# Kernel tuning notes

Hardware: AMD Instinct MI355X
Metric: run time of the kernel (lower is better)

The kernel has to match this reference:

```python
import jax, jax.numpy as jnp
import numpy as np

NUM_ITER = 3
SLOT_DIM = 16
INPUT_DIM = 256
HIDDEN_DIM = 128
EPS = 1e-8
LN_EPS = 1e-5  # torch LayerNorm default


def _layernorm(x, w, b):
    mu = jnp.mean(x, axis=-1, keepdims=True)
    var = jnp.mean((x - mu) ** 2, axis=-1, keepdims=True)
    return (x - mu) * jax.lax.rsqrt(var + LN_EPS) * w + b


def setup_inputs() -> dict:
    key = jax.random.key(0)
    ks = jax.random.split(key, 12)
    B, N, K = 32, 4096, 8
    D, S, H = INPUT_DIM, SLOT_DIM, HIDDEN_DIM
    inputs = jax.random.normal(ks[0], (B, N, D), dtype=jnp.float32)
    init_slots = jax.random.normal(ks[1], (B, K, S), dtype=jnp.float32)
    return {
        "inputs": inputs,
        "init_slots": init_slots,
        "ln_in_w": jnp.ones((D,), jnp.float32),
        "ln_in_b": jnp.zeros((D,), jnp.float32),
        "ln_s_w": jnp.ones((S,), jnp.float32),
        "ln_s_b": jnp.zeros((S,), jnp.float32),
        "ln_m_w": jnp.ones((S,), jnp.float32),
        "ln_m_b": jnp.zeros((S,), jnp.float32),
        "wq": jax.random.normal(ks[2], (S, S), jnp.float32) * (S ** -0.5),
        "wk": jax.random.normal(ks[3], (S, D), jnp.float32) * (D ** -0.5),
        "wv": jax.random.normal(ks[4], (S, D), jnp.float32) * (D ** -0.5),
        "w_ih": jax.random.normal(ks[5], (3 * S, S), jnp.float32) * (S ** -0.5),
        "w_hh": jax.random.normal(ks[6], (3 * S, S), jnp.float32) * (S ** -0.5),
        "b_ih": jnp.zeros((3 * S,), jnp.float32),
        "b_hh": jnp.zeros((3 * S,), jnp.float32),
        "mlp_w1": jax.random.normal(ks[7], (H, S), jnp.float32) * (S ** -0.5),
        "mlp_b1": jnp.zeros((H,), jnp.float32),
        "mlp_w2": jax.random.normal(ks[8], (S, H), jnp.float32) * (H ** -0.5),
        "mlp_b2": jnp.zeros((S,), jnp.float32),
    }


def _gru_cell(x, h, w_ih, w_hh, b_ih, b_hh):
    # torch GRUCell: gates ordered [r, z, n]
    gi = x @ w_ih.T + b_ih            # [BK, 3S]
    gh = h @ w_hh.T + b_hh
    i_r, i_z, i_n = jnp.split(gi, 3, axis=-1)
    h_r, h_z, h_n = jnp.split(gh, 3, axis=-1)
    r = jax.nn.sigmoid(i_r + h_r)
    z = jax.nn.sigmoid(i_z + h_z)
    n = jnp.tanh(i_n + r * h_n)
    return (1.0 - z) * n + z * h


def reference(inputs, init_slots, ln_in_w, ln_in_b, ln_s_w, ln_s_b, ln_m_w, ln_m_b,
              wq, wk, wv, w_ih, w_hh, b_ih, b_hh, mlp_w1, mlp_b1, mlp_w2, mlp_b2):
    B, N, _ = inputs.shape
    K = init_slots.shape[1]
    scale = SLOT_DIM ** -0.5

    x = _layernorm(inputs, ln_in_w, ln_in_b)
    k = jnp.einsum('bnd,sd->bns', x, wk)   # [B,N,S]
    v = jnp.einsum('bnd,sd->bns', x, wv)

    slots = init_slots
    attn = None
    for _ in range(NUM_ITER):
        slots_prev = slots
        q = jnp.einsum('bks,ts->bkt', _layernorm(slots, ln_s_w, ln_s_b), wq)
        logits = jnp.einsum('bks,bns->bkn', q, k) * scale       # [B,K,N]
        attn = jax.nn.softmax(logits, axis=1) + EPS              # softmax over SLOTS
        attn = attn / jnp.sum(attn, axis=-1, keepdims=True)
        updates = jnp.einsum('bkn,bns->bks', attn, v)            # [B,K,S]
        h = _gru_cell(updates.reshape(B * K, -1), slots_prev.reshape(B * K, -1),
                      w_ih, w_hh, b_ih, b_hh).reshape(B, K, -1)
        y = _layernorm(h, ln_m_w, ln_m_b)
        mlp = jax.nn.relu(y @ mlp_w1.T + mlp_b1) @ mlp_w2.T + mlp_b2
        slots = h + mlp
    return slots, attn
```

## Files before the change

kernel.cpp:

```cpp
#include <hip/hip_runtime.h>
#include <cstddef>


__device__ __forceinline__ float sigmoid_f(float x){ return 1.f/(1.f+__expf(-x)); }
__device__ __forceinline__ float tanh_f(float x){ return 1.f - 2.f/(__expf(2.f*x)+1.f); }

__global__ __launch_bounds__(256) void k_prep(
    const float* __restrict__ lnw, const float* __restrict__ lnb,
    const float* __restrict__ wk, const float* __restrict__ wv,
    const float* __restrict__ init_slots,
    const float* __restrict__ ln_s_w, const float* __restrict__ ln_s_b,
    const float* __restrict__ wq,
    float* __restrict__ wprepT, float* __restrict__ mt,
    float* __restrict__ qbuf, float* __restrict__ upd, float* __restrict__ Abuf,
    float* __restrict__ slots_out)
{
  int t = threadIdx.x;
  int i = blockIdx.x*256 + t;
  {
    int j = i & 15, s = (i >> 4) & 31, c = (i >> 9) & 3, p = i >> 11;
    int d = p*64 + c*16 + j;
    float w = (s < 16) ? wk[s*256+d] : wv[(s-16)*256+d];
    wprepT[i] = lnw[d]*w;
  }
  if (blockIdx.x != 0) return;
  {
    int s = t >> 3, j = t & 7;
    float m = 0.f, tv = 0.f;
    for (int d = j; d < 256; d += 8) {
      float w = (s < 16) ? wk[s*256+d] : wv[(s-16)*256+d];
      m  = fmaf(lnw[d], w, m);
      tv = fmaf(lnb[d], w, tv);
    }
    m += __shfl_xor(m,1);  m += __shfl_xor(m,2);  m += __shfl_xor(m,4);
    tv += __shfl_xor(tv,1); tv += __shfl_xor(tv,2); tv += __shfl_xor(tv,4);
    if (j == 0) { mt[s] = m; mt[32+s] = tv; }
  }
  #pragma unroll
  for (int j2 = 0; j2 < 16; ++j2) {
    slots_out[t*16+j2] = init_slots[t*16+j2];
    upd[t*16+j2] = 0.f;
  }
  Abuf[t] = 0.f;
  float sl[16];
  #pragma unroll
  for (int j2 = 0; j2 < 16; ++j2) sl[j2] = init_slots[t*16+j2];
  float mu = 0.f;
  #pragma unroll
  for (int j2 = 0; j2 < 16; ++j2) mu += sl[j2];
  mu *= (1.f/16.f);
  float var = 0.f;
  #pragma unroll
  for (int j2 = 0; j2 < 16; ++j2) { float d = sl[j2]-mu; var = fmaf(d,d,var); }
  var *= (1.f/16.f);
  float rstd = rsqrtf(var + 1e-5f);
  float y[16];
  #pragma unroll
  for (int j2 = 0; j2 < 16; ++j2) y[j2] = (sl[j2]-mu)*rstd*ln_s_w[j2] + ln_s_b[j2];
  #pragma unroll
  for (int tq = 0; tq < 16; ++tq) {
    float q = 0.f;
    #pragma unroll
    for (int s2 = 0; s2 < 16; ++s2) q = fmaf(y[s2], wq[tq*16+s2], q);
    qbuf[t*16+tq] = q;
  }
}

__global__ __launch_bounds__(256) void k_proj(
    const float* __restrict__ x, const float* __restrict__ wprepT,
    const float* __restrict__ mt,
    float* __restrict__ kout, float* __restrict__ vout)
{
  __shared__ float pbuf[4][64][35];
  int t = threadIdx.x;
  int lane = t & 63;
  int p = __builtin_amdgcn_readfirstlane(t >> 6);
  int row = blockIdx.x*64 + lane;
  const float* xr = x + (size_t)row*256 + p*64;
  const float* wp = wprepT + p*2048;

  float acc[32];
  #pragma unroll
  for (int s = 0; s < 32; ++s) acc[s] = 0.f;
  float sum = 0.f, sumsq = 0.f;

  float4 n0 = *(const float4*)(xr+0);
  float4 n1 = *(const float4*)(xr+4);
  float4 n2 = *(const float4*)(xr+8);
  float4 n3 = *(const float4*)(xr+12);
  #pragma unroll 1
  for (int c = 0; c < 4; ++c) {
    float4 x0 = n0, x1 = n1, x2 = n2, x3 = n3;
    if (c < 3) {
      const float* xn = xr + (c+1)*16;
      n0 = *(const float4*)(xn+0);
      n1 = *(const float4*)(xn+4);
      n2 = *(const float4*)(xn+8);
      n3 = *(const float4*)(xn+12);
    }
    float xe[16] = {x0.x,x0.y,x0.z,x0.w, x1.x,x1.y,x1.z,x1.w,
                    x2.x,x2.y,x2.z,x2.w, x3.x,x3.y,x3.z,x3.w};
    #pragma unroll
    for (int j = 0; j < 16; ++j) { sum += xe[j]; sumsq = fmaf(xe[j], xe[j], sumsq); }
    const float* wc = wp + c*512;
    #pragma unroll
    for (int s = 0; s < 32; ++s) {
      const float* w = wc + s*16;
      #pragma unroll
      for (int j = 0; j < 16; ++j) acc[s] = fmaf(xe[j], w[j], acc[s]);
    }
  }
  #pragma unroll
  for (int s = 0; s < 32; ++s) pbuf[p][lane][s] = acc[s];
  pbuf[p][lane][32] = sum;
  pbuf[p][lane][33] = sumsq;
  __syncthreads();

  int g = t >> 6, r = t & 63;
  float ts = 0.f, tq = 0.f;
  #pragma unroll
  for (int pp = 0; pp < 4; ++pp) { ts += pbuf[pp][r][32]; tq += pbuf[pp][r][33]; }
  float mu = ts*(1.f/256.f);
  float var = tq*(1.f/256.f) - mu*mu;
  float rstd = rsqrtf(var + 1e-5f);
  float o[8];
  #pragma unroll
  for (int j = 0; j < 8; ++j) {
    int a = g*8 + j;
    float v = 0.f;
    #pragma unroll
    for (int pp = 0; pp < 4; ++pp) v += pbuf[pp][r][a];
    o[j] = fmaf(rstd, v - mu*mt[a], mt[32+a]);
  }
  float* dst = ((g < 2) ? kout : vout) + (size_t)(blockIdx.x*64 + r)*16 + (g & 1)*8;
  *(float4*)(dst+0) = make_float4(o[0],o[1],o[2],o[3]);
  *(float4*)(dst+4) = make_float4(o[4],o[5],o[6],o[7]);
}

__global__ __launch_bounds__(256) void k_attn(
    const float* __restrict__ kproj, const float* __restrict__ vproj,
    const float* __restrict__ qbuf,
    float* __restrict__ upd, float* __restrict__ Abuf,
    float* __restrict__ attn_out, int write_attn)
{
  __shared__ float qs[128];
  __shared__ float ptile[8*257];
  __shared__ float vtile[16*257];
  int b = blockIdx.x >> 4;
  int n0 = (blockIdx.x & 15) * 256;
  int t = threadIdx.x;
  if (t < 128) qs[t] = qbuf[b*128 + t];

  float kv[16];
  {
    const float* kr = kproj + ((size_t)(b*4096 + n0 + t))*16;
    const float* vr = vproj + ((size_t)(b*4096 + n0 + t))*16;
    #pragma unroll
    for (int j = 0; j < 16; j += 4) {
      float4 f = *(const float4*)(kr+j);
      kv[j]=f.x; kv[j+1]=f.y; kv[j+2]=f.z; kv[j+3]=f.w;
      float4 g = *(const float4*)(vr+j);
      vtile[(j+0)*257+t]=g.x; vtile[(j+1)*257+t]=g.y;
      vtile[(j+2)*257+t]=g.z; vtile[(j+3)*257+t]=g.w;
    }
  }
  __syncthreads();
  {
    float lg[8];
    #pragma unroll
    for (int kk = 0; kk < 8; ++kk) {
      float a = 0.f;
      #pragma unroll
      for (int s = 0; s < 16; ++s) a = fmaf(qs[kk*16+s], kv[s], a);
      lg[kk] = a*0.25f;
    }
    float mx = lg[0];
    #pragma unroll
    for (int kk = 1; kk < 8; ++kk) mx = fmaxf(mx, lg[kk]);
    float se = 0.f;
    #pragma unroll
    for (int kk = 0; kk < 8; ++kk) { lg[kk] = __expf(lg[kk]-mx); se += lg[kk]; }
    float inv = 1.f/se;
    #pragma unroll
    for (int kk = 0; kk < 8; ++kk) {
      float pv = fmaf(lg[kk], inv, 1e-8f);
      ptile[kk*257 + t] = pv;
      if (write_attn) attn_out[((size_t)(b*8+kk))*4096 + n0 + t] = pv;
    }
  }
  __syncthreads();
  {
    int kk = t >> 5, r = t & 31, s = r >> 1, half = r & 1;
    const float* pr = ptile + kk*257 + half*128;
    const float* vr = vtile + s*257 + half*128;
    float acc = 0.f, asum = 0.f;
    #pragma unroll 8
    for (int i = 0; i < 128; ++i) {
      float pv = pr[i];
      asum += pv;
      acc = fmaf(pv, vr[i], acc);
    }
    acc  += __shfl_xor(acc, 1);
    asum += __shfl_xor(asum, 1);
    if (half == 0) {
      atomicAdd(upd + (b*8+kk)*16 + s, acc);
      if (s == 0) atomicAdd(Abuf + b*8 + kk, asum);
    }
  }
}

__global__ __launch_bounds__(256) void k_gru(
    float* __restrict__ upd, float* __restrict__ Abuf,
    float* __restrict__ slots, float* __restrict__ qbuf,
    const float* __restrict__ w_ih, const float* __restrict__ w_hh,
    const float* __restrict__ b_ih, const float* __restrict__ b_hh,
    const float* __restrict__ mlp_w1, const float* __restrict__ mlp_b1,
    const float* __restrict__ mlp_w2, const float* __restrict__ mlp_b2,
    const float* __restrict__ ln_m_w, const float* __restrict__ ln_m_b,
    const float* __restrict__ ln_s_w, const float* __restrict__ ln_s_b,
    const float* __restrict__ wq, int prep_next)
{
  __shared__ float s_wih[48*17], s_whh[48*17];
  __shared__ float s_bih[48], s_bhh[48];
  __shared__ float s_w1[128*17], s_b1[128];
  __shared__ float s_w2[16*129], s_b2[16];
  __shared__ float s_lnmw[16], s_lnmb[16], s_lnsw[16], s_lnsb[16];
  __shared__ float s_wq[16*17];
  int t = threadIdx.x;
  for (int i = t; i < 768; i += 256) {
    int g = i >> 4, j = i & 15;
    s_wih[g*17+j] = w_ih[i];
    s_whh[g*17+j] = w_hh[i];
  }
  for (int i = t; i < 2048; i += 256) {
    int r = i >> 4, c = i & 15;
    s_w1[r*17+c] = mlp_w1[i];
    int r2 = i >> 7, c2 = i & 127;
    s_w2[r2*129+c2] = mlp_w2[i];
  }
  if (t < 48) { s_bih[t] = b_ih[t]; s_bhh[t] = b_hh[t]; }
  if (t < 128) s_b1[t] = mlp_b1[t];
  if (t < 16) {
    s_b2[t] = mlp_b2[t];
    s_lnmw[t] = ln_m_w[t]; s_lnmb[t] = ln_m_b[t];
    s_lnsw[t] = ln_s_w[t]; s_lnsb[t] = ln_s_b[t];
  }
  for (int i = t; i < 256; i += 256) {
    int r = i >> 4, c = i & 15;
    s_wq[r*17+c] = wq[i];
  }
  __syncthreads();

  int bk = blockIdx.x*16 + (t >> 4);
  int s = t & 15;
  int laneBase = (t & 63) & ~15;

  float inv = 1.f / Abuf[bk];
  float u[16], h[16];
  #pragma unroll
  for (int j = 0; j < 16; ++j) {
    u[j] = upd[bk*16+j] * inv;
    h[j] = slots[bk*16+j];
  }
  float hs = slots[bk*16+s];

  float gir = s_bih[s],  giz = s_bih[16+s], gin = s_bih[32+s];
  float ghr = s_bhh[s],  ghz = s_bhh[16+s], ghn = s_bhh[32+s];
  #pragma unroll
  for (int j = 0; j < 16; ++j) {
    gir = fmaf(u[j], s_wih[s*17+j], gir);
    giz = fmaf(u[j], s_wih[(16+s)*17+j], giz);
    gin = fmaf(u[j], s_wih[(32+s)*17+j], gin);
    ghr = fmaf(h[j], s_whh[s*17+j], ghr);
    ghz = fmaf(h[j], s_whh[(16+s)*17+j], ghz);
    ghn = fmaf(h[j], s_whh[(32+s)*17+j], ghn);
  }
  float rr = sigmoid_f(gir + ghr);
  float zz = sigmoid_f(giz + ghz);
  float nn = tanh_f(gin + rr*ghn);
  float hn = (1.f-zz)*nn + zz*hs;

  float ssum = hn;
  #pragma unroll
  for (int m = 1; m < 16; m <<= 1) ssum += __shfl_xor(ssum, m);
  float mu = ssum*(1.f/16.f);
  float dv = hn - mu;
  float vs = dv*dv;
  #pragma unroll
  for (int m = 1; m < 16; m <<= 1) vs += __shfl_xor(vs, m);
  float rstd = rsqrtf(vs*(1.f/16.f) + 1e-5f);
  float y = dv*rstd*s_lnmw[s] + s_lnmb[s];

  float yv[16];
  #pragma unroll
  for (int j = 0; j < 16; ++j) yv[j] = __shfl(y, laneBase + j);

  float h1[8];
  #pragma unroll
  for (int i = 0; i < 8; ++i) {
    int jj = i*16 + s;
    float a = s_b1[jj];
    #pragma unroll
    for (int q = 0; q < 16; ++q) a = fmaf(yv[q], s_w1[jj*17+q], a);
    h1[i] = fmaxf(a, 0.f);
  }
  float o = s_b2[s];
  #pragma unroll
  for (int i = 0; i < 8; ++i) {
    #pragma unroll
    for (int sp = 0; sp < 16; ++sp) {
      float hv = __shfl(h1[i], laneBase + sp);
      o = fmaf(hv, s_w2[s*129 + i*16 + sp], o);
    }
  }
  float slot_new = hn + o;
  slots[bk*16+s] = slot_new;

  if (prep_next) {
    float ss = slot_new;
    #pragma unroll
    for (int m = 1; m < 16; m <<= 1) ss += __shfl_xor(ss, m);
    float mu2 = ss*(1.f/16.f);
    float d2 = slot_new - mu2;
    float v2 = d2*d2;
    #pragma unroll
    for (int m = 1; m < 16; m <<= 1) v2 += __shfl_xor(v2, m);
    float rstd2 = rsqrtf(v2*(1.f/16.f) + 1e-5f);
    float y2 = d2*rstd2*s_lnsw[s] + s_lnsb[s];
    float qv = 0.f;
    #pragma unroll
    for (int sp = 0; sp < 16; ++sp) qv = fmaf(__shfl(y2, laneBase+sp), s_wq[s*17+sp], qv);
    qbuf[bk*16+s] = qv;
    upd[bk*16+s] = 0.f;
    if (s == 0) Abuf[bk] = 0.f;
  }
}

__global__ __launch_bounds__(256) void k_scale(float* __restrict__ attn,
                                               const float* __restrict__ Abuf)
{
  int bk = blockIdx.x;
  float inv = 1.f / Abuf[bk];
  float4* p = (float4*)(attn + (size_t)bk*4096);
  #pragma unroll 4
  for (int i = threadIdx.x; i < 1024; i += 256) {
    float4 v = p[i];
    v.x *= inv; v.y *= inv; v.z *= inv; v.w *= inv;
    p[i] = v;
  }
}

extern "C" void kernel_launch(void* const* d_in, const int* in_sizes, int n_in,
                              void* d_out, int out_size, void* d_ws, size_t ws_size,
                              hipStream_t stream)
{
  const float* inputs     = (const float*)d_in[0];
  const float* init_slots = (const float*)d_in[1];
  const float* ln_in_w    = (const float*)d_in[2];
  const float* ln_in_b    = (const float*)d_in[3];
  const float* ln_s_w     = (const float*)d_in[4];
  const float* ln_s_b     = (const float*)d_in[5];
  const float* ln_m_w     = (const float*)d_in[6];
  const float* ln_m_b     = (const float*)d_in[7];
  const float* wq         = (const float*)d_in[8];
  const float* wk         = (const float*)d_in[9];
  const float* wv         = (const float*)d_in[10];
  const float* w_ih       = (const float*)d_in[11];
  const float* w_hh       = (const float*)d_in[12];
  const float* b_ih       = (const float*)d_in[13];
  const float* b_hh       = (const float*)d_in[14];
  const float* mlp_w1     = (const float*)d_in[15];
  const float* mlp_b1     = (const float*)d_in[16];
  const float* mlp_w2     = (const float*)d_in[17];
  const float* mlp_b2     = (const float*)d_in[18];

  float* ws    = (float*)d_ws;
  float* wprepT= ws;
  float* mt    = ws + 8192;
  float* qbuf  = ws + 8320;
  float* upd   = ws + 12416;
  float* Abuf  = ws + 16512;
  float* kproj = ws + 16768;
  float* vproj = kproj + 2097152;

  float* out   = (float*)d_out;
  float* slots = out;
  float* attn  = out + 4096;

  k_prep<<<32, 256, 0, stream>>>(ln_in_w, ln_in_b, wk, wv, init_slots,
                                 ln_s_w, ln_s_b, wq,
                                 wprepT, mt, qbuf, upd, Abuf, slots);
  k_proj<<<2048, 256, 0, stream>>>(inputs, wprepT, mt, kproj, vproj);
  for (int it = 0; it < 3; ++it) {
    int last = (it == 2);
    k_attn<<<512, 256, 0, stream>>>(kproj, vproj, qbuf, upd, Abuf, attn, last);
    k_gru<<<16, 256, 0, stream>>>(upd, Abuf, slots, qbuf,
                                  w_ih, w_hh, b_ih, b_hh,
                                  mlp_w1, mlp_b1, mlp_w2, mlp_b2,
                                  ln_m_w, ln_m_b, ln_s_w, ln_s_b,
                                  wq, last ? 0 : 1);
  }
  k_scale<<<256, 256, 0, stream>>>(attn, Abuf);
}
```

Before: 320.2 us.

## Stage input rows through LDS with coalesced loads in projection and attention kernels

The projection kernel now loads x tiles cooperatively with coalesced float4 reads into shared memory, double-buffered through registers, instead of having each thread stride its own row. The weight layout is reordered to match. The attention kernel stages k through an LDS tile with coalesced loads and vectorizes the dot products and the p·v reduction with float4 LDS reads using padded strides. This targets uncoalesced global access and scalar LDS traffic, at the cost of extra barriers per chunk.

```diff
diff --git a/kernel.cpp b/kernel.cpp
--- a/kernel.cpp
+++ b/kernel.cpp
@@ -18,8 +18,8 @@
   int t = threadIdx.x;
   int i = blockIdx.x*256 + t;
   {
-    int j = i & 15, s = (i >> 4) & 31, c = (i >> 9) & 3, p = i >> 11;
-    int d = p*64 + c*16 + j;
+    int j = i & 15, s = (i >> 4) & 31, g = i >> 9;
+    int d = g*16 + j;
     float w = (s < 16) ? wk[s*256+d] : wv[(s-16)*256+d];
     wprepT[i] = lnw[d]*w;
   }
@@ -71,55 +71,70 @@
     const float* __restrict__ mt,
     float* __restrict__ kout, float* __restrict__ vout)
 {
-  __shared__ float pbuf[4][64][35];
+  __shared__ float smem[8960];
+  float* xs = smem;
+  float* pb = smem;
   int t = threadIdx.x;
   int lane = t & 63;
   int p = __builtin_amdgcn_readfirstlane(t >> 6);
-  int row = blockIdx.x*64 + lane;
-  const float* xr = x + (size_t)row*256 + p*64;
-  const float* wp = wprepT + p*2048;
+  int r0 = blockIdx.x*64;
+  int srow = t >> 4, scol = (t & 15)*4;
 
   float acc[32];
   #pragma unroll
   for (int s = 0; s < 32; ++s) acc[s] = 0.f;
   float sum = 0.f, sumsq = 0.f;
 
-  float4 n0 = *(const float4*)(xr+0);
-  float4 n1 = *(const float4*)(xr+4);
-  float4 n2 = *(const float4*)(xr+8);
-  float4 n3 = *(const float4*)(xr+12);
+  float4 st[4];
+  #pragma unroll
+  for (int i = 0; i < 4; ++i)
+    st[i] = *(const float4*)(x + (size_t)(r0 + i*16 + srow)*256 + 0*64 + scol);
+  #pragma unroll
+  for (int i = 0; i < 4; ++i)
+    *(float4*)&xs[(i*16 + srow)*68 + scol] = st[i];
+  __syncthreads();
+
   #pragma unroll 1
   for (int c = 0; c < 4; ++c) {
-    float4 x0 = n0, x1 = n1, x2 = n2, x3 = n3;
     if (c < 3) {
-      const float* xn = xr + (c+1)*16;
-      n0 = *(const float4*)(xn+0);
-      n1 = *(const float4*)(xn+4);
-      n2 = *(const float4*)(xn+8);
-      n3 = *(const float4*)(xn+12);
-    }
-    float xe[16] = {x0.x,x0.y,x0.z,x0.w, x1.x,x1.y,x1.z,x1.w,
-                    x2.x,x2.y,x2.z,x2.w, x3.x,x3.y,x3.z,x3.w};
+      #pragma unroll
+      for (int i = 0; i < 4; ++i)
+        st[i] = *(const float4*)(x + (size_t)(r0 + i*16 + srow)*256 + (c+1)*64 + scol);
+    }
+    float xe[16];
+    #pragma unroll
+    for (int i = 0; i < 4; ++i) {
+      float4 f = *(const float4*)&xs[lane*68 + p*16 + i*4];
+      xe[i*4+0]=f.x; xe[i*4+1]=f.y; xe[i*4+2]=f.z; xe[i*4+3]=f.w;
+    }
     #pragma unroll
     for (int j = 0; j < 16; ++j) { sum += xe[j]; sumsq = fmaf(xe[j], xe[j], sumsq); }
-    const float* wc = wp + c*512;
+    const float* wc = wprepT + (c*4 + p)*512;
     #pragma unroll
     for (int s = 0; s < 32; ++s) {
       const float* w = wc + s*16;
       #pragma unroll
       for (int j = 0; j < 16; ++j) acc[s] = fmaf(xe[j], w[j], acc[s]);
     }
-  }
-  #pragma unroll
-  for (int s = 0; s < 32; ++s) pbuf[p][lane][s] = acc[s];
-  pbuf[p][lane][32] = sum;
-  pbuf[p][lane][33] = sumsq;
+    __syncthreads();
+    if (c < 3) {
+      #pragma unroll
+      for (int i = 0; i < 4; ++i)
+        *(float4*)&xs[(i*16 + srow)*68 + scol] = st[i];
+      __syncthreads();
+    }
+  }
+
+  #pragma unroll
+  for (int s = 0; s < 32; ++s) pb[(p*64 + lane)*35 + s] = acc[s];
+  pb[(p*64 + lane)*35 + 32] = sum;
+  pb[(p*64 + lane)*35 + 33] = sumsq;
   __syncthreads();
 
   int g = t >> 6, r = t & 63;
   float ts = 0.f, tq = 0.f;
   #pragma unroll
-  for (int pp = 0; pp < 4; ++pp) { ts += pbuf[pp][r][32]; tq += pbuf[pp][r][33]; }
+  for (int pp = 0; pp < 4; ++pp) { ts += pb[(pp*64+r)*35 + 32]; tq += pb[(pp*64+r)*35 + 33]; }
   float mu = ts*(1.f/256.f);
   float var = tq*(1.f/256.f) - mu*mu;
   float rstd = rsqrtf(var + 1e-5f);
@@ -129,10 +144,10 @@
     int a = g*8 + j;
     float v = 0.f;
     #pragma unroll
-    for (int pp = 0; pp < 4; ++pp) v += pbuf[pp][r][a];
+    for (int pp = 0; pp < 4; ++pp) v += pb[(pp*64+r)*35 + a];
     o[j] = fmaf(rstd, v - mu*mt[a], mt[32+a]);
   }
-  float* dst = ((g < 2) ? kout : vout) + (size_t)(blockIdx.x*64 + r)*16 + (g & 1)*8;
+  float* dst = ((g < 2) ? kout : vout) + (size_t)(r0 + r)*16 + (g & 1)*8;
   *(float4*)(dst+0) = make_float4(o[0],o[1],o[2],o[3]);
   *(float4*)(dst+4) = make_float4(o[4],o[5],o[6],o[7]);
 }
@@ -144,35 +159,50 @@
     float* __restrict__ attn_out, int write_attn)
 {
   __shared__ float qs[128];
-  __shared__ float ptile[8*257];
-  __shared__ float vtile[16*257];
+  __shared__ float ktile[256*20];
+  __shared__ float vtile[16*260];
+  __shared__ float ptile[8*260];
   int b = blockIdx.x >> 4;
   int n0 = (blockIdx.x & 15) * 256;
   int t = threadIdx.x;
+
+  const float* kbase = kproj + ((size_t)(b*4096 + n0))*16;
+  const float* vbase = vproj + ((size_t)(b*4096 + n0))*16;
+  {
+    int nn = t >> 2, s0 = (t & 3)*4;
+    #pragma unroll
+    for (int i = 0; i < 4; ++i) {
+      int n = i*64 + nn;
+      float4 kf = *(const float4*)(kbase + n*16 + s0);
+      *(float4*)&ktile[n*20 + s0] = kf;
+      float4 vf = *(const float4*)(vbase + n*16 + s0);
+      vtile[(s0+0)*260 + n] = vf.x;
+      vtile[(s0+1)*260 + n] = vf.y;
+      vtile[(s0+2)*260 + n] = vf.z;
+      vtile[(s0+3)*260 + n] = vf.w;
+    }
+  }
   if (t < 128) qs[t] = qbuf[b*128 + t];
-
-  float kv[16];
+  __syncthreads();
+
   {
-    const float* kr = kproj + ((size_t)(b*4096 + n0 + t))*16;
-    const float* vr = vproj + ((size_t)(b*4096 + n0 + t))*16;
-    #pragma unroll
-    for (int j = 0; j < 16; j += 4) {
-      float4 f = *(const float4*)(kr+j);
-      kv[j]=f.x; kv[j+1]=f.y; kv[j+2]=f.z; kv[j+3]=f.w;
-      float4 g = *(const float4*)(vr+j);
-      vtile[(j+0)*257+t]=g.x; vtile[(j+1)*257+t]=g.y;
-      vtile[(j+2)*257+t]=g.z; vtile[(j+3)*257+t]=g.w;
-    }
-  }
-  __syncthreads();
-  {
+    float4 kv[4];
+    #pragma unroll
+    for (int i = 0; i < 4; ++i) kv[i] = *(const float4*)&ktile[t*20 + i*4];
+    const float4* q4 = (const float4*)qs;
     float lg[8];
     #pragma unroll
     for (int kk = 0; kk < 8; ++kk) {
-      float a = 0.f;
+      float4 a4 = make_float4(0.f,0.f,0.f,0.f);
       #pragma unroll
-      for (int s = 0; s < 16; ++s) a = fmaf(qs[kk*16+s], kv[s], a);
-      lg[kk] = a*0.25f;
+      for (int i = 0; i < 4; ++i) {
+        float4 q = q4[kk*4+i];
+        a4.x = fmaf(q.x, kv[i].x, a4.x);
+        a4.y = fmaf(q.y, kv[i].y, a4.y);
+        a4.z = fmaf(q.z, kv[i].z, a4.z);
+        a4.w = fmaf(q.w, kv[i].w, a4.w);
+      }
+      lg[kk] = ((a4.x+a4.y)+(a4.z+a4.w))*0.25f;
     }
     float mx = lg[0];
     #pragma unroll
@@ -184,22 +214,28 @@
     #pragma unroll
     for (int kk = 0; kk < 8; ++kk) {
       float pv = fmaf(lg[kk], inv, 1e-8f);
-      ptile[kk*257 + t] = pv;
+      ptile[kk*260 + t] = pv;
       if (write_attn) attn_out[((size_t)(b*8+kk))*4096 + n0 + t] = pv;
     }
   }
   __syncthreads();
   {
     int kk = t >> 5, r = t & 31, s = r >> 1, half = r & 1;
-    const float* pr = ptile + kk*257 + half*128;
-    const float* vr = vtile + s*257 + half*128;
-    float acc = 0.f, asum = 0.f;
+    const float4* pr = (const float4*)(ptile + kk*260 + half*128);
+    const float4* vr = (const float4*)(vtile + s*260 + half*128);
+    float4 a4 = make_float4(0.f,0.f,0.f,0.f);
+    float4 s4 = make_float4(0.f,0.f,0.f,0.f);
     #pragma unroll 8
-    for (int i = 0; i < 128; ++i) {
-      float pv = pr[i];
-      asum += pv;
-      acc = fmaf(pv, vr[i], acc);
-    }
+    for (int i = 0; i < 32; ++i) {
+      float4 pv = pr[i], vv = vr[i];
+      s4.x += pv.x; s4.y += pv.y; s4.z += pv.z; s4.w += pv.w;
+      a4.x = fmaf(pv.x, vv.x, a4.x);
+      a4.y = fmaf(pv.y, vv.y, a4.y);
+      a4.z = fmaf(pv.z, vv.z, a4.z);
+      a4.w = fmaf(pv.w, vv.w, a4.w);
+    }
+    float acc  = (a4.x+a4.y)+(a4.z+a4.w);
+    float asum = (s4.x+s4.y)+(s4.z+s4.w);
     acc  += __shfl_xor(acc, 1);
     asum += __shfl_xor(asum, 1);
     if (half == 0) {
```

Result: slower. 361.6 us (+12.9%).
